# Performance work log

Measured on AMD Instinct MI355X. Metric: run time of the kernel, lower is better.

## Reference

```python
import jax, jax.numpy as jnp
import numpy as np

EPS = 1e-8


def _three_nn_interpolate(coords, ref_coords, features):
    # coords: [B, N, 3], ref_coords: [B, M, 3], features: [B, C, M]
    # squared pairwise distances [B, N, M]
    d2 = (
        jnp.sum(coords * coords, axis=-1, keepdims=True)          # [B, N, 1]
        + jnp.sum(ref_coords * ref_coords, axis=-1)[:, None, :]    # [B, 1, M]
        - 2.0 * jnp.einsum('bnd,bmd->bnm', coords, ref_coords)
    )
    neg_d, idx = jax.lax.top_k(-d2, 3)       # 3 nearest -> idx [B, N, 3]
    dist = -neg_d                             # squared dists of 3-NN
    w = 1.0 / (dist + EPS)
    w = w / jnp.sum(w, axis=-1, keepdims=True)  # [B, N, 3]
    feats_t = jnp.swapaxes(features, 1, 2)    # [B, M, C]
    gathered = jax.vmap(lambda f, i: f[i])(feats_t, idx)  # [B, N, 3, C]
    out = jnp.einsum('bnk,bnkc->bcn', w, gathered)         # [B, C, N]
    return out


def setup_inputs() -> dict:
    key = jax.random.key(0)
    ks = jax.random.split(key, 5)
    B, N, M = 2, 16384, 4096
    return {
        'coords': jax.random.normal(ks[0], (B, N, 3), dtype=jnp.float32),
        'ref_coords': jax.random.normal(ks[1], (B, M, 3), dtype=jnp.float32),
        'ref_features': jax.random.normal(ks[2], (B, 256, M), dtype=jnp.float32),
        'ref_t_embed': jax.random.normal(ks[3], (B, 128, M), dtype=jnp.float32),
        'points_features': jax.random.normal(ks[4], (B, 64, N), dtype=jnp.float32),
    }


def reference(coords, ref_coords, ref_features, ref_t_embed, points_features):
    # PointNetFPModule.forward: interpolate features and t_embed from the
    # coarse ref point set onto the dense point set, then concat skip features.
    features = _three_nn_interpolate(coords, ref_coords, ref_features)  # [B, 256, N]
    t_embed = _three_nn_interpolate(coords, ref_coords, ref_t_embed)    # [B, 128, N]
    features = jnp.concatenate([features, points_features], axis=1)     # [B, 320, N]
    return features, t_embed
```

## Files before the change

kernel.cpp:

```cpp
#include <hip/hip_runtime.h>
#include <cstdint>

#define BB 2
#define NN 16384
#define MM 4096
#define CF 256
#define CT 128
#define CP 64

#define TPB1 512
#define NPB1 64
#define CHUNK 2048

__global__ __launch_bounds__(TPB1, 4) void knn_kernel(
    const float* __restrict__ coords,
    const float* __restrict__ ref_coords,
    int4* __restrict__ wsI,
    float4* __restrict__ wsW)
{
#pragma clang fp contract(off)
    __shared__ float4 refs[CHUNK];

    const int tid = threadIdx.x;
    const int b   = blockIdx.y;
    const int n0  = blockIdx.x * NPB1;

    const int pl = tid >> 4;
    const int s  = tid & 15;
    const int nA = n0 + pl * 2;

    const float* cp = coords + ((size_t)b * NN + nA) * 3;
    const float ax = cp[0], ay = cp[1], az = cp[2];
    const float bx = cp[3], by = cp[4], bz = cp[5];
    const float acc_ = (ax * ax + ay * ay) + az * az;
    const float bcc_ = (bx * bx + by * by) + bz * bz;

    float aD0 = INFINITY, aD1 = INFINITY, aD2 = INFINITY;
    float bD0 = INFINITY, bD1 = INFINITY, bD2 = INFINITY;
    int   aI0 = 0, aI1 = 0, aI2 = 0;
    int   bI0 = 0, bI1 = 0, bI2 = 0;

    const float* rc = ref_coords + (size_t)b * MM * 3;

    for (int ch = 0; ch < MM / CHUNK; ++ch) {
        __syncthreads();
        for (int e = tid; e < CHUNK; e += TPB1) {
            const int j = ch * CHUNK + e;
            const float x = rc[3 * j + 0];
            const float y = rc[3 * j + 1];
            const float z = rc[3 * j + 2];
            refs[e] = make_float4(x + x, y + y, z + z, (x * x + y * y) + z * z);
        }
        __syncthreads();

        const float4* rp = &refs[s];
        const int jb0 = ch * CHUNK + s;
        for (int kb = 0; kb < CHUNK / 16 / 32; ++kb) {
            const float4* rpb = rp + (size_t)kb * 32 * 16;
            const int jbb = jb0 + (kb * 32) * 16;
            #pragma unroll
            for (int k = 0; k < 32; ++k) {
                const float4 r = rpb[k * 16];
                const int j = jbb + k * 16;
                {
                    const float dot2 = (ax * r.x + ay * r.y) + az * r.z;
                    const float dd   = (acc_ + r.w) - dot2;
                    const bool l2 = dd < aD2;
                    const bool l1 = dd < aD1;
                    const bool l0 = dd < aD0;
                    aI2 = l2 ? (l1 ? aI1 : j) : aI2;
                    aI1 = l1 ? (l0 ? aI0 : j) : aI1;
                    aI0 = l0 ? j : aI0;
                    const float n2  = __builtin_amdgcn_fmed3f(dd, aD1, aD2);
                    const float n1  = __builtin_amdgcn_fmed3f(dd, aD0, aD1);
                    const float n0v = fminf(dd, aD0);
                    aD2 = n2; aD1 = n1; aD0 = n0v;
                }
                {
                    const float dot2 = (bx * r.x + by * r.y) + bz * r.z;
                    const float dd   = (bcc_ + r.w) - dot2;
                    const bool l2 = dd < bD2;
                    const bool l1 = dd < bD1;
                    const bool l0 = dd < bD0;
                    bI2 = l2 ? (l1 ? bI1 : j) : bI2;
                    bI1 = l1 ? (l0 ? bI0 : j) : bI1;
                    bI0 = l0 ? j : bI0;
                    const float n2  = __builtin_amdgcn_fmed3f(dd, bD1, bD2);
                    const float n1  = __builtin_amdgcn_fmed3f(dd, bD0, bD1);
                    const float n0v = fminf(dd, bD0);
                    bD2 = n2; bD1 = n1; bD0 = n0v;
                }
            }
        }
    }

    for (int off = 1; off < 16; off <<= 1) {
        {
            const float e0 = __shfl_xor(aD0, off, 64);
            const float e1 = __shfl_xor(aD1, off, 64);
            const float e2 = __shfl_xor(aD2, off, 64);
            const int   f0 = __shfl_xor(aI0, off, 64);
            const int   f1 = __shfl_xor(aI1, off, 64);
            const int   f2 = __shfl_xor(aI2, off, 64);
            auto ins = [&](float e, int f) {
                const bool l2 = (e < aD2) || (e == aD2 && f < aI2);
                const bool l1 = (e < aD1) || (e == aD1 && f < aI1);
                const bool l0 = (e < aD0) || (e == aD0 && f < aI0);
                aD2 = l2 ? (l1 ? aD1 : e) : aD2;  aI2 = l2 ? (l1 ? aI1 : f) : aI2;
                aD1 = l1 ? (l0 ? aD0 : e) : aD1;  aI1 = l1 ? (l0 ? aI0 : f) : aI1;
                aD0 = l0 ? e : aD0;               aI0 = l0 ? f : aI0;
            };
            ins(e0, f0); ins(e1, f1); ins(e2, f2);
        }
        {
            const float e0 = __shfl_xor(bD0, off, 64);
            const float e1 = __shfl_xor(bD1, off, 64);
            const float e2 = __shfl_xor(bD2, off, 64);
            const int   f0 = __shfl_xor(bI0, off, 64);
            const int   f1 = __shfl_xor(bI1, off, 64);
            const int   f2 = __shfl_xor(bI2, off, 64);
            auto ins = [&](float e, int f) {
                const bool l2 = (e < bD2) || (e == bD2 && f < bI2);
                const bool l1 = (e < bD1) || (e == bD1 && f < bI1);
                const bool l0 = (e < bD0) || (e == bD0 && f < bI0);
                bD2 = l2 ? (l1 ? bD1 : e) : bD2;  bI2 = l2 ? (l1 ? bI1 : f) : bI2;
                bD1 = l1 ? (l0 ? bD0 : e) : bD1;  bI1 = l1 ? (l0 ? bI0 : f) : bI1;
                bD0 = l0 ? e : bD0;               bI0 = l0 ? f : bI0;
            };
            ins(e0, f0); ins(e1, f1); ins(e2, f2);
        }
    }

    if (s == 0) {
        {
            float w0 = 1.0f / (aD0 + 1e-8f);
            float w1 = 1.0f / (aD1 + 1e-8f);
            float w2 = 1.0f / (aD2 + 1e-8f);
            const float sum = (w0 + w1) + w2;
            wsI[(size_t)b * NN + nA] = make_int4(aI0, aI1, aI2, 0);
            wsW[(size_t)b * NN + nA] = make_float4(w0 / sum, w1 / sum, w2 / sum, 0.0f);
        }
        {
            float w0 = 1.0f / (bD0 + 1e-8f);
            float w1 = 1.0f / (bD1 + 1e-8f);
            float w2 = 1.0f / (bD2 + 1e-8f);
            const float sum = (w0 + w1) + w2;
            wsI[(size_t)b * NN + nA + 1] = make_int4(bI0, bI1, bI2, 0);
            wsW[(size_t)b * NN + nA + 1] = make_float4(w0 / sum, w1 / sum, w2 / sum, 0.0f);
        }
    }
}

#define TPB2 512
#define NIB  (BB * (CF + CT) / 2)
#define NCB  32

__global__ __launch_bounds__(TPB2, 8) void interp_kernel(
    const float* __restrict__ refF,
    const float* __restrict__ refT,
    const float* __restrict__ pf,
    const int4*  __restrict__ wsI,
    const float4* __restrict__ wsW,
    float* __restrict__ out)
{
#pragma clang fp contract(off)
    __shared__ float rowA[MM];
    __shared__ float rowB[MM];
    const int tid  = threadIdx.x;
    const int task = blockIdx.x;
    const size_t outT_base = (size_t)BB * (CF + CP) * NN;

    if (task >= NIB) {
        const int t3 = task - NIB;
        for (int j = 0; j < 4; ++j) {
            const int r  = t3 * 4 + j;
            const int bb = r >> 6;
            const int c  = r & (CP - 1);
            const float4* s4 = (const float4*)(pf + ((size_t)bb * CP + c) * NN);
            float4* d4 = (float4*)(out + ((size_t)bb * (CF + CP) + CF + c) * NN);
            for (int i = tid; i < NN / 4; i += TPB2) d4[i] = s4[i];
        }
        return;
    }

    const int r0 = task * 2;
    const float* src0;
    float* dst0;
    int b;
    if (r0 < BB * CF) {
        b = r0 >> 8;
        const int c = r0 & (CF - 1);
        src0 = refF + ((size_t)b * CF + c) * MM;
        dst0 = out + ((size_t)b * (CF + CP) + c) * NN;
    } else {
        const int r2 = r0 - BB * CF;
        b = r2 >> 7;
        const int c = r2 & (CT - 1);
        src0 = refT + ((size_t)b * CT + c) * MM;
        dst0 = out + outT_base + ((size_t)b * CT + c) * NN;
    }
    const float* src1 = src0 + MM;
    float* dst1 = dst0 + NN;

    for (int i = tid; i < MM / 4; i += TPB2) {
        ((float4*)rowA)[i] = ((const float4*)src0)[i];
        ((float4*)rowB)[i] = ((const float4*)src1)[i];
    }
    __syncthreads();

    const int4*   wi = wsI + (size_t)b * NN;
    const float4* ww = wsW + (size_t)b * NN;

    auto clampi = [](int v) { return v < 0 ? 0 : (v > MM - 1 ? MM - 1 : v); };

    int4   id = wi[tid];
    float4 w  = ww[tid];
    for (int nq = tid; nq < NN; nq += TPB2) {
        const int nq2 = nq + TPB2;
        int4   idn;
        float4 wn;
        if (nq2 < NN) { idn = wi[nq2]; wn = ww[nq2]; }
        const int a0 = clampi(id.x), a1 = clampi(id.y), a2 = clampi(id.z);
        dst0[nq] = (w.x * rowA[a0] + w.y * rowA[a1]) + w.z * rowA[a2];
        dst1[nq] = (w.x * rowB[a0] + w.y * rowB[a1]) + w.z * rowB[a2];
        id = idn; w = wn;
    }
}

extern "C" void kernel_launch(void* const* d_in, const int* in_sizes, int n_in,
                              void* d_out, int out_size, void* d_ws, size_t ws_size,
                              hipStream_t stream) {
    const float* coords     = (const float*)d_in[0];
    const float* ref_coords = (const float*)d_in[1];
    const float* refF       = (const float*)d_in[2];
    const float* refT       = (const float*)d_in[3];
    const float* pf         = (const float*)d_in[4];
    float* out = (float*)d_out;

    int4*   wsI = (int4*)d_ws;
    float4* wsW = (float4*)((char*)d_ws + (size_t)BB * NN * sizeof(int4));

    hipLaunchKernelGGL(knn_kernel, dim3(NN / NPB1, BB), dim3(TPB1), 0, stream,
                       coords, ref_coords, wsI, wsW);
    hipLaunchKernelGGL(interp_kernel, dim3(NIB + NCB), dim3(TPB2), 0, stream,
                       refF, refT, pf, wsI, wsW, out);
}
```

Baseline: 182.9 us.

## Prune 3-NN candidates with wave-level threshold vote from lane-group tau

Each group of 16 lanes shares its worst-kept distance: every 32 candidates, a shuffle reduction takes the minimum third-best distance across those lanes. Candidates whose distance is not below min(own third-best, shared tau) cannot reach the global top 3, so the whole insert sequence is skipped whenever `__any` finds no lane with a qualifying candidate. This targets the compare/select/med3 insertion work that runs for every reference point. In exchange it adds a per-element wave vote and branch, plus a periodic shuffle reduction, and lowers the unroll from 32 to 4. Ties at the threshold could resolve differently from the full merge.

```diff
diff --git a/kernel.cpp b/kernel.cpp
--- a/kernel.cpp
+++ b/kernel.cpp
@@ -39,6 +39,8 @@
     float bD0 = INFINITY, bD1 = INFINITY, bD2 = INFINITY;
     int   aI0 = 0, aI1 = 0, aI2 = 0;
     int   bI0 = 0, bI1 = 0, bI2 = 0;
+    float tauA = INFINITY, tauB = INFINITY;
+    float thrA = INFINITY, thrB = INFINITY;
 
     const float* rc = ref_coords + (size_t)b * MM * 3;
 
@@ -53,44 +55,58 @@
         }
         __syncthreads();
 
-        const float4* rp = &refs[s];
-        const int jb0 = ch * CHUNK + s;
-        for (int kb = 0; kb < CHUNK / 16 / 32; ++kb) {
-            const float4* rpb = rp + (size_t)kb * 32 * 16;
-            const int jbb = jb0 + (kb * 32) * 16;
-            #pragma unroll
+        const int jbase = ch * CHUNK;
+        for (int it0 = 0; it0 < CHUNK / 16; it0 += 32) {
+            #pragma unroll 4
             for (int k = 0; k < 32; ++k) {
-                const float4 r = rpb[k * 16];
-                const int j = jbb + k * 16;
-                {
-                    const float dot2 = (ax * r.x + ay * r.y) + az * r.z;
-                    const float dd   = (acc_ + r.w) - dot2;
-                    const bool l2 = dd < aD2;
-                    const bool l1 = dd < aD1;
-                    const bool l0 = dd < aD0;
-                    aI2 = l2 ? (l1 ? aI1 : j) : aI2;
-                    aI1 = l1 ? (l0 ? aI0 : j) : aI1;
-                    aI0 = l0 ? j : aI0;
-                    const float n2  = __builtin_amdgcn_fmed3f(dd, aD1, aD2);
-                    const float n1  = __builtin_amdgcn_fmed3f(dd, aD0, aD1);
-                    const float n0v = fminf(dd, aD0);
-                    aD2 = n2; aD1 = n1; aD0 = n0v;
-                }
-                {
-                    const float dot2 = (bx * r.x + by * r.y) + bz * r.z;
-                    const float dd   = (bcc_ + r.w) - dot2;
-                    const bool l2 = dd < bD2;
-                    const bool l1 = dd < bD1;
-                    const bool l0 = dd < bD0;
-                    bI2 = l2 ? (l1 ? bI1 : j) : bI2;
-                    bI1 = l1 ? (l0 ? bI0 : j) : bI1;
-                    bI0 = l0 ? j : bI0;
-                    const float n2  = __builtin_amdgcn_fmed3f(dd, bD1, bD2);
-                    const float n1  = __builtin_amdgcn_fmed3f(dd, bD0, bD1);
-                    const float n0v = fminf(dd, bD0);
-                    bD2 = n2; bD1 = n1; bD0 = n0v;
+                const int e = s + ((it0 + k) << 4);
+                const float4 r = refs[e];
+                const float dotA = (ax * r.x + ay * r.y) + az * r.z;
+                const float ddA  = (acc_ + r.w) - dotA;
+                const float dotB = (bx * r.x + by * r.y) + bz * r.z;
+                const float ddB  = (bcc_ + r.w) - dotB;
+                if (__any((ddA < thrA) || (ddB < thrB))) {
+                    const int j = jbase + e;
+                    {
+                        const bool l2 = ddA < aD2;
+                        const bool l1 = ddA < aD1;
+                        const bool l0 = ddA < aD0;
+                        aI2 = l2 ? (l1 ? aI1 : j) : aI2;
+                        aI1 = l1 ? (l0 ? aI0 : j) : aI1;
+                        aI0 = l0 ? j : aI0;
+                        const float n2  = __builtin_amdgcn_fmed3f(ddA, aD1, aD2);
+                        const float n1  = __builtin_amdgcn_fmed3f(ddA, aD0, aD1);
+                        const float n0v = fminf(ddA, aD0);
+                        aD2 = n2; aD1 = n1; aD0 = n0v;
+                    }
+                    {
+                        const bool l2 = ddB < bD2;
+                        const bool l1 = ddB < bD1;
+                        const bool l0 = ddB < bD0;
+                        bI2 = l2 ? (l1 ? bI1 : j) : bI2;
+                        bI1 = l1 ? (l0 ? bI0 : j) : bI1;
+                        bI0 = l0 ? j : bI0;
+                        const float n2  = __builtin_amdgcn_fmed3f(ddB, bD1, bD2);
+                        const float n1  = __builtin_amdgcn_fmed3f(ddB, bD0, bD1);
+                        const float n0v = fminf(ddB, bD0);
+                        bD2 = n2; bD1 = n1; bD0 = n0v;
+                    }
+                    thrA = fminf(aD2, tauA);
+                    thrB = fminf(bD2, tauB);
                 }
             }
+            float tA = aD2, tB = bD2;
+            tA = fminf(tA, __shfl_xor(tA, 1, 64));
+            tB = fminf(tB, __shfl_xor(tB, 1, 64));
+            tA = fminf(tA, __shfl_xor(tA, 2, 64));
+            tB = fminf(tB, __shfl_xor(tB, 2, 64));
+            tA = fminf(tA, __shfl_xor(tA, 4, 64));
+            tB = fminf(tB, __shfl_xor(tB, 4, 64));
+            tA = fminf(tA, __shfl_xor(tA, 8, 64));
+            tB = fminf(tB, __shfl_xor(tB, 8, 64));
+            tauA = tA;  tauB = tB;
+            thrA = fminf(aD2, tauA);
+            thrB = fminf(bD2, tauB);
         }
     }
 
```

Result: slower. 191.2 us (+4.5%).
